# Optimization experiments

Hardware: AMD Instinct MI355X
Metric: run time of the kernel (lower is better)

The kernel has to match this reference:

```python
import jax, jax.numpy as jnp
import numpy as np

VOCAB = 50257
EMBED = 256
HIDDEN = 128
NUM_CLASSES = 2
BATCH = 128
SEQ = 1024


def setup_inputs() -> dict:
    key = jax.random.key(0)
    ks = jax.random.split(key, 8)
    x = jax.random.randint(ks[0], (BATCH, SEQ), 0, VOCAB, dtype=jnp.int32).astype(jnp.int64)
    emb = jax.random.normal(ks[1], (VOCAB, EMBED), dtype=jnp.float32)
    emb = emb.at[0].set(0.0)  # padding_idx=0 row is zeros
    s = 1.0 / np.sqrt(HIDDEN)  # torch LSTM/Linear init scale
    W_ih = jax.random.uniform(ks[2], (4 * HIDDEN, EMBED), minval=-s, maxval=s, dtype=jnp.float32)
    W_hh = jax.random.uniform(ks[3], (4 * HIDDEN, HIDDEN), minval=-s, maxval=s, dtype=jnp.float32)
    b_ih = jax.random.uniform(ks[4], (4 * HIDDEN,), minval=-s, maxval=s, dtype=jnp.float32)
    b_hh = jax.random.uniform(ks[5], (4 * HIDDEN,), minval=-s, maxval=s, dtype=jnp.float32)
    W_fc = jax.random.uniform(ks[6], (NUM_CLASSES, HIDDEN), minval=-s, maxval=s, dtype=jnp.float32)
    b_fc = jax.random.uniform(ks[7], (NUM_CLASSES,), minval=-s, maxval=s, dtype=jnp.float32)
    return {"x": x, "emb": emb, "W_ih": W_ih, "W_hh": W_hh,
            "b_ih": b_ih, "b_hh": b_hh, "W_fc": W_fc, "b_fc": b_fc}


def reference(x, emb, W_ih, W_hh, b_ih, b_hh, W_fc, b_fc):
    # Embedding lookup: [B, T, E]
    embedded = emb[x]
    # Precompute input-to-hidden gate projections for all timesteps: [B, T, 4H]
    xg = jnp.einsum('bte,ge->btg', embedded, W_ih) + (b_ih + b_hh)
    B = x.shape[0]
    h0 = jnp.zeros((B, HIDDEN), dtype=emb.dtype)
    c0 = jnp.zeros((B, HIDDEN), dtype=emb.dtype)

    def step(carry, xt):
        h, c = carry
        gates = xt + h @ W_hh.T  # [B, 4H]
        i, f, g, o = jnp.split(gates, 4, axis=-1)  # torch gate order: i, f, g, o
        i = jax.nn.sigmoid(i)
        f = jax.nn.sigmoid(f)
        g = jnp.tanh(g)
        o = jax.nn.sigmoid(o)
        c = f * c + i * g
        h = o * jnp.tanh(c)
        return (h, c), None

    (h_T, c_T), _ = jax.lax.scan(step, (h0, c0), jnp.swapaxes(xg, 0, 1))
    # dropout is identity at inference; final linear head
    return h_T @ W_fc.T + b_fc
```

## Files before the change

kernel.cpp:

```cpp
#include <hip/hip_runtime.h>
#include <hip/hip_bf16.h>

#define VOCAB 50257
#define EMBED 256
#define HIDDEN 128
#define G4 512
#define BATCH 128
#define SEQ 1024

typedef float f32x4 __attribute__((ext_vector_type(4)));

__device__ __forceinline__ float dpp_xor1(float x) {
    return __int_as_float(__builtin_amdgcn_update_dpp(
        0, __float_as_int(x), 0xB1 , 0xF, 0xF, true));
}
__device__ __forceinline__ float dpp_xor2(float x) {
    return __int_as_float(__builtin_amdgcn_update_dpp(
        0, __float_as_int(x), 0x4E , 0xF, 0xF, true));
}

#define K1_BM 128
#define K1_BN 64
#define K1_BK 32

__global__ __launch_bounds__(256)
void table_gemm(const float* __restrict__ emb, const float* __restrict__ Wih,
                const float* __restrict__ bih, const float* __restrict__ bhh,
                float* __restrict__ table) {
    __shared__ __align__(16) float As[K1_BK][K1_BM + 4];
    __shared__ __align__(16) float Bs[K1_BK][K1_BN + 4];

    const int nTiles = G4 / K1_BN;
    const int mt = blockIdx.x / nTiles;
    const int nt = blockIdx.x % nTiles;
    const int m0 = mt * K1_BM, n0 = nt * K1_BN;
    const int tid  = threadIdx.x;
    const int tm   = tid & 15;
    const int tn   = tid >> 4;
    const int lrow = tid >> 3;
    const int lk   = (tid & 7) << 2;

    float acc[8][4];
#pragma unroll
    for (int i = 0; i < 8; ++i)
#pragma unroll
        for (int j = 0; j < 4; ++j) acc[i][j] = 0.f;

    for (int k0 = 0; k0 < EMBED; k0 += K1_BK) {
        __syncthreads();
#pragma unroll
        for (int p = 0; p < 4; ++p) {
            int m  = m0 + p * 32 + lrow;
            int ms = m < VOCAB ? m : VOCAB - 1;
            f32x4 a = *(const f32x4*)(emb + (size_t)ms * EMBED + k0 + lk);
            As[lk + 0][p * 32 + lrow] = a[0];
            As[lk + 1][p * 32 + lrow] = a[1];
            As[lk + 2][p * 32 + lrow] = a[2];
            As[lk + 3][p * 32 + lrow] = a[3];
        }
#pragma unroll
        for (int p = 0; p < 2; ++p) {
            int n = n0 + p * 32 + lrow;
            f32x4 b = *(const f32x4*)(Wih + (size_t)n * EMBED + k0 + lk);
            Bs[lk + 0][p * 32 + lrow] = b[0];
            Bs[lk + 1][p * 32 + lrow] = b[1];
            Bs[lk + 2][p * 32 + lrow] = b[2];
            Bs[lk + 3][p * 32 + lrow] = b[3];
        }
        __syncthreads();
#pragma unroll
        for (int k = 0; k < K1_BK; ++k) {
            f32x4 b4   = *(const f32x4*)&Bs[k][tn * 4];
            f32x4 a4lo = *(const f32x4*)&As[k][tm * 8];
            f32x4 a4hi = *(const f32x4*)&As[k][tm * 8 + 4];
#pragma unroll
            for (int i = 0; i < 4; ++i)
#pragma unroll
                for (int j = 0; j < 4; ++j) {
                    acc[i][j]     += a4lo[i] * b4[j];
                    acc[i + 4][j] += a4hi[i] * b4[j];
                }
        }
    }

    const int nbase = n0 + tn * 4;
    float bias0 = bih[nbase + 0] + bhh[nbase + 0];
    float bias1 = bih[nbase + 1] + bhh[nbase + 1];
    float bias2 = bih[nbase + 2] + bhh[nbase + 2];
    float bias3 = bih[nbase + 3] + bhh[nbase + 3];
#pragma unroll
    for (int i = 0; i < 8; ++i) {
        int m = m0 + tm * 8 + i;
        if (m < VOCAB) {
            f32x4 o;
            o[0] = acc[i][0] + bias0;
            o[1] = acc[i][1] + bias1;
            o[2] = acc[i][2] + bias2;
            o[3] = acc[i][3] + bias3;
            *(f32x4*)(table + (size_t)m * G4 + nbase) = o;
        }
    }
}

__global__ __launch_bounds__(512, 2)
void lstm_seq(const int* __restrict__ x, const float* __restrict__ table,
              const float* __restrict__ Whh,
              const float* __restrict__ Wfc, const float* __restrict__ bfc,
              float* __restrict__ out) {
    __shared__ __align__(16) float h_s[2][HIDDEN];
    __shared__ int toks[SEQ];

    const int b   = blockIdx.x;
    const int tid = threadIdx.x;
    const int i4  = tid & 3;
    const int Q   = tid >> 2;

    for (int t = tid; t < SEQ; t += 512) toks[t] = x[b * SEQ + t];

    f32x4 wv[4][8];
#pragma unroll
    for (int g = 0; g < 4; ++g)
#pragma unroll
        for (int j = 0; j < 8; ++j)
            wv[g][j] = *(const f32x4*)(Whh + (size_t)(g * HIDDEN + Q) * HIDDEN
                                           + 32 * i4 + 4 * (j ^ (2 * i4)));

    if (tid < HIDDEN) h_s[0][tid] = 0.f;
    float c = 0.f;
    const int lane_off = i4 * HIDDEN + Q;
    __syncthreads();

    float xg_cur = table[(size_t)toks[0] * G4 + lane_off];
    float xg_nxt = table[(size_t)toks[1] * G4 + lane_off];

    for (int t = 0; t < SEQ; ++t) {
        int   tk2   = toks[(t + 2) & (SEQ - 1)];
        float xg_n2 = table[(size_t)tk2 * G4 + lane_off];

        const float* hb = h_s[t & 1];
        f32x4 hc[8];
#pragma unroll
        for (int j = 0; j < 8; ++j)
            hc[j] = *(const f32x4*)(hb + 32 * i4 + 4 * (j ^ (2 * i4)));

        f32x4 a0 = {0.f,0.f,0.f,0.f}, a1 = {0.f,0.f,0.f,0.f};
        f32x4 a2 = {0.f,0.f,0.f,0.f}, a3 = {0.f,0.f,0.f,0.f};
#pragma unroll
        for (int j = 0; j < 8; ++j) {
            a0 += wv[0][j] * hc[j];
            a1 += wv[1][j] * hc[j];
            a2 += wv[2][j] * hc[j];
            a3 += wv[3][j] * hc[j];
        }
        float p0 = (a0[0] + a0[1]) + (a0[2] + a0[3]);
        float p1 = (a1[0] + a1[1]) + (a1[2] + a1[3]);
        float p2 = (a2[0] + a2[1]) + (a2[2] + a2[3]);
        float p3 = (a3[0] + a3[1]) + (a3[2] + a3[3]);
        p0 += (i4 == 0) ? xg_cur : 0.f;
        p1 += (i4 == 1) ? xg_cur : 0.f;
        p2 += (i4 == 2) ? xg_cur : 0.f;
        p3 += (i4 == 3) ? xg_cur : 0.f;

        float u0 = p0 + dpp_xor1(p0);
        float u1 = p1 + dpp_xor1(p1);
        float u2 = p2 + dpp_xor1(p2);
        float u3 = p3 + dpp_xor1(p3);
        float v0 = (i4 & 1) ? u2 : u0;
        float v1 = (i4 & 1) ? u3 : u1;
        float w0 = v0 + dpp_xor2(v0);
        float w1 = v1 + dpp_xor2(v1);
        float o0 = dpp_xor1(w0);
        float o1 = dpp_xor1(w1);
        float gi = (i4 & 1) ? o0 : w0;
        float gf = (i4 & 1) ? o1 : w1;
        float gg = (i4 & 1) ? w0 : o0;
        float go = (i4 & 1) ? w1 : o1;

        float si = __builtin_amdgcn_rcpf(1.f + __expf(-gi));
        float sf = __builtin_amdgcn_rcpf(1.f + __expf(-gf));
        float so = __builtin_amdgcn_rcpf(1.f + __expf(-go));
        float eg = __expf(2.f * gg);
        float tg = 1.f - 2.f * __builtin_amdgcn_rcpf(eg + 1.f);
        c = sf * c + si * tg;
        float ec = __expf(2.f * c);
        float tc = 1.f - 2.f * __builtin_amdgcn_rcpf(ec + 1.f);
        float h  = so * tc;

        if (i4 == 0) h_s[(t + 1) & 1][Q] = h;
        __syncthreads();

        xg_cur = xg_nxt;
        xg_nxt = xg_n2;
    }

    if (tid < 2) {
        const f32x4* wf = (const f32x4*)(Wfc + tid * HIDDEN);
        const f32x4* h4 = (const f32x4*)h_s[0];
        f32x4 s = {0.f, 0.f, 0.f, 0.f};
#pragma unroll
        for (int k = 0; k < 32; ++k) s += wf[k] * h4[k];
        out[b * 2 + tid] = bfc[tid] + ((s[0] + s[1]) + (s[2] + s[3]));
    }
}

extern "C" void kernel_launch(void* const* d_in, const int* in_sizes, int n_in,
                              void* d_out, int out_size, void* d_ws, size_t ws_size,
                              hipStream_t stream) {
    (void)in_sizes; (void)n_in; (void)out_size; (void)ws_size;
    const int*   x   = (const int*)d_in[0];
    const float* emb = (const float*)d_in[1];
    const float* Wih = (const float*)d_in[2];
    const float* Whh = (const float*)d_in[3];
    const float* bih = (const float*)d_in[4];
    const float* bhh = (const float*)d_in[5];
    const float* Wfc = (const float*)d_in[6];
    const float* bfc = (const float*)d_in[7];
    float* out   = (float*)d_out;
    float* table = (float*)d_ws;

    const int mTiles = (VOCAB + K1_BM - 1) / K1_BM;
    const int nTiles = G4 / K1_BN;
    table_gemm<<<dim3(mTiles * nTiles), 256, 0, stream>>>(emb, Wih, bih, bhh, table);
    lstm_seq<<<dim3(BATCH), 512, 0, stream>>>(x, table, Whh, Wfc, bfc, out);
}
```

Baseline: 932.7 us.

## Halve LSTM block threads so each quad computes two hidden units

The recurrent kernel now uses 256 threads per sequence instead of 512, with each group of four lanes computing all four gates for two hidden units. Each thread holds twice as many W_hh rows in registers and loads two gate-input values as a pair. The DPP reduction is reorganised so gate values land directly on lanes 0/1 without the final swap. This is meant to cut barrier and wave-scheduling cost per timestep, at the price of doubled per-thread FMA work and much higher register pressure.

Result: slower. 1.353 ms (+45.1%).

```diff
diff --git a/kernel.cpp b/kernel.cpp
--- a/kernel.cpp
+++ b/kernel.cpp
@@ -9,6 +9,7 @@
 #define SEQ 1024
 
 typedef float f32x4 __attribute__((ext_vector_type(4)));
+typedef float f32x2 __attribute__((ext_vector_type(2)));
 
 __device__ __forceinline__ float dpp_xor1(float x) {
     return __int_as_float(__builtin_amdgcn_update_dpp(
@@ -102,7 +103,7 @@
     }
 }
 
-__global__ __launch_bounds__(512, 2)
+__global__ __launch_bounds__(256, 1)
 void lstm_seq(const int* __restrict__ x, const float* __restrict__ table,
               const float* __restrict__ Whh,
               const float* __restrict__ Wfc, const float* __restrict__ bfc,
@@ -112,69 +113,69 @@
 
     const int b   = blockIdx.x;
     const int tid = threadIdx.x;
-    const int i4  = tid & 3;
+    const int j   = tid & 3;
     const int Q   = tid >> 2;
 
-    for (int t = tid; t < SEQ; t += 512) toks[t] = x[b * SEQ + t];
-
-    f32x4 wv[4][8];
-#pragma unroll
-    for (int g = 0; g < 4; ++g)
-#pragma unroll
-        for (int j = 0; j < 8; ++j)
-            wv[g][j] = *(const f32x4*)(Whh + (size_t)(g * HIDDEN + Q) * HIDDEN
-                                           + 32 * i4 + 4 * (j ^ (2 * i4)));
+    for (int t = tid; t < SEQ; t += 256) toks[t] = x[b * SEQ + t];
+
+    f32x4 wv[8][8];
+#pragma unroll
+    for (int m = 0; m < 8; ++m) {
+        const float* wrow = Whh + (size_t)((m & 3) * HIDDEN + 2 * Q + (m >> 2)) * HIDDEN;
+#pragma unroll
+        for (int r = 0; r < 8; ++r)
+            wv[m][r] = *(const f32x4*)(wrow + 32 * j + 4 * (r ^ (2 * j)));
+    }
 
     if (tid < HIDDEN) h_s[0][tid] = 0.f;
     float c = 0.f;
-    const int lane_off = i4 * HIDDEN + Q;
+    const int xgoff = j * HIDDEN + 2 * Q;
     __syncthreads();
 
-    float xg_cur = table[(size_t)toks[0] * G4 + lane_off];
-    float xg_nxt = table[(size_t)toks[1] * G4 + lane_off];
+    f32x2 xg_cur = *(const f32x2*)(table + (size_t)toks[0] * G4 + xgoff);
+    f32x2 xg_nxt = *(const f32x2*)(table + (size_t)toks[1] * G4 + xgoff);
 
     for (int t = 0; t < SEQ; ++t) {
-        int   tk2   = toks[(t + 2) & (SEQ - 1)];
-        float xg_n2 = table[(size_t)tk2 * G4 + lane_off];
+        int   tk2    = toks[(t + 2) & (SEQ - 1)];
+        f32x2 xg_n2  = *(const f32x2*)(table + (size_t)tk2 * G4 + xgoff);
 
         const float* hb = h_s[t & 1];
         f32x4 hc[8];
 #pragma unroll
-        for (int j = 0; j < 8; ++j)
-            hc[j] = *(const f32x4*)(hb + 32 * i4 + 4 * (j ^ (2 * i4)));
-
-        f32x4 a0 = {0.f,0.f,0.f,0.f}, a1 = {0.f,0.f,0.f,0.f};
-        f32x4 a2 = {0.f,0.f,0.f,0.f}, a3 = {0.f,0.f,0.f,0.f};
-#pragma unroll
-        for (int j = 0; j < 8; ++j) {
-            a0 += wv[0][j] * hc[j];
-            a1 += wv[1][j] * hc[j];
-            a2 += wv[2][j] * hc[j];
-            a3 += wv[3][j] * hc[j];
-        }
-        float p0 = (a0[0] + a0[1]) + (a0[2] + a0[3]);
-        float p1 = (a1[0] + a1[1]) + (a1[2] + a1[3]);
-        float p2 = (a2[0] + a2[1]) + (a2[2] + a2[3]);
-        float p3 = (a3[0] + a3[1]) + (a3[2] + a3[3]);
-        p0 += (i4 == 0) ? xg_cur : 0.f;
-        p1 += (i4 == 1) ? xg_cur : 0.f;
-        p2 += (i4 == 2) ? xg_cur : 0.f;
-        p3 += (i4 == 3) ? xg_cur : 0.f;
-
-        float u0 = p0 + dpp_xor1(p0);
-        float u1 = p1 + dpp_xor1(p1);
-        float u2 = p2 + dpp_xor1(p2);
-        float u3 = p3 + dpp_xor1(p3);
-        float v0 = (i4 & 1) ? u2 : u0;
-        float v1 = (i4 & 1) ? u3 : u1;
-        float w0 = v0 + dpp_xor2(v0);
-        float w1 = v1 + dpp_xor2(v1);
-        float o0 = dpp_xor1(w0);
-        float o1 = dpp_xor1(w1);
-        float gi = (i4 & 1) ? o0 : w0;
-        float gf = (i4 & 1) ? o1 : w1;
-        float gg = (i4 & 1) ? w0 : o0;
-        float go = (i4 & 1) ? w1 : o1;
+        for (int r = 0; r < 8; ++r)
+            hc[r] = *(const f32x4*)(hb + 32 * j + 4 * (r ^ (2 * j)));
+
+        f32x4 a[8];
+#pragma unroll
+        for (int m = 0; m < 8; ++m) a[m] = (f32x4){0.f, 0.f, 0.f, 0.f};
+#pragma unroll
+        for (int r = 0; r < 8; ++r)
+#pragma unroll
+            for (int m = 0; m < 8; ++m)
+                a[m] += wv[m][r] * hc[r];
+
+        float p[8];
+#pragma unroll
+        for (int m = 0; m < 8; ++m)
+            p[m] = (a[m][0] + a[m][1]) + (a[m][2] + a[m][3]);
+#pragma unroll
+        for (int m = 0; m < 4; ++m) {
+            p[m]     += (j == m) ? xg_cur[0] : 0.f;
+            p[m + 4] += (j == m) ? xg_cur[1] : 0.f;
+        }
+
+        float u[8];
+#pragma unroll
+        for (int m = 0; m < 8; ++m) u[m] = p[m] + dpp_xor1(p[m]);
+        const bool hi = (j & 1);
+        float v0 = hi ? u[4] : u[0];
+        float v1 = hi ? u[5] : u[1];
+        float v2 = hi ? u[6] : u[2];
+        float v3 = hi ? u[7] : u[3];
+        float gi = v0 + dpp_xor2(v0);
+        float gf = v1 + dpp_xor2(v1);
+        float gg = v2 + dpp_xor2(v2);
+        float go = v3 + dpp_xor2(v3);
 
         float si = __builtin_amdgcn_rcpf(1.f + __expf(-gi));
         float sf = __builtin_amdgcn_rcpf(1.f + __expf(-gf));
@@ -186,7 +187,8 @@
         float tc = 1.f - 2.f * __builtin_amdgcn_rcpf(ec + 1.f);
         float h  = so * tc;
 
-        if (i4 == 0) h_s[(t + 1) & 1][Q] = h;
+        const int nxt = (t + 1) & 1;
+        if (j < 2) h_s[nxt][2 * Q + j] = h;
         __syncthreads();
 
         xg_cur = xg_nxt;
@@ -221,5 +223,5 @@
     const int mTiles = (VOCAB + K1_BM - 1) / K1_BM;
     const int nTiles = G4 / K1_BN;
     table_gemm<<<dim3(mTiles * nTiles), 256, 0, stream>>>(emb, Wih, bih, bhh, table);
-    lstm_seq<<<dim3(BATCH), 512, 0, stream>>>(x, table, Whh, Wfc, bfc, out);
-}
+    lstm_seq<<<dim3(BATCH), 256, 0, stream>>>(x, table, Whh, Wfc, bfc, out);
+}
```
